# Optimization experiments

Hardware: AMD Instinct MI355X
Metric: run time of the kernel (lower is better)

The kernel has to match this reference:

```python
import jax, jax.numpy as jnp
from jax import lax
import numpy as np

# dims (match init_kwargs config)
B, L, D = 32, 512, 32          # batch, seq_len, input_dim
H = 256                         # hidden_dim
E = 8                           # num_experts
PLEN, O = 96, 32                # pred_len, output_dim
LAT = 256                       # flow latent_dim
PD, NPROT = 64, 16              # prototype_dim, num_prototypes


def setup_inputs() -> dict:
    key = jax.random.key(0)
    ks = iter(jax.random.split(key, 40))
    def n(shape, scale=0.02):
        return (jax.random.normal(next(ks), shape, jnp.float32) * scale)
    inp = {
        'x': jax.random.normal(next(ks), (B, L, D), jnp.float32),
        # prototypes + projector (metric gating / diversity)
        'prototypes': n((NPROT, PD), 0.5),
        'Wp': n((PD, PD)), 'bp': jnp.zeros((PD,), jnp.float32),
        # expert_feature_extractor: Linear(7D->H), ReLU, Linear(H->PD), LayerNorm(PD)
        'Wf1': n((7 * D, H)), 'bf1': jnp.zeros((H,), jnp.float32),
        'Wf2': n((H, PD)), 'bf2': jnp.zeros((PD,), jnp.float32),
        'ln_g': jnp.ones((PD,), jnp.float32), 'ln_b': jnp.zeros((PD,), jnp.float32),
        # flow encoder (latent mapping of flattened window) + gating head
        'W1': n((L * D, H)), 'b1': jnp.zeros((H,), jnp.float32),
        'W2': n((H, LAT)), 'b2': jnp.zeros((LAT,), jnp.float32),
        'Wg': n((LAT, E)), 'bg': jnp.zeros((E,), jnp.float32),
        'log_temp': jnp.zeros((), jnp.float32),
        # stacked FFT+Mamba expert params (leading axis = expert)
        'Win': n((E, D, H)), 'b_in': jnp.zeros((E, H), jnp.float32),
        'Wfft': n((E, H, H)), 'b_fft': jnp.zeros((E, H), jnp.float32),
        'a_logit': n((E, H), 1.0),
        'Whead': n((E, H, PLEN * O)), 'b_head': jnp.zeros((E, PLEN * O), jnp.float32),
    }
    return inp


def _expert_features(x, Wf1, bf1, Wf2, bf2, ln_g, ln_b):
    # faithful to compute_expert_features: 7 per-channel stats -> MLP -> LayerNorm
    Lf = jnp.float32(x.shape[1])
    x_mean = x.mean(axis=1)
    x_std = x.std(axis=1, ddof=1)             # torch unbiased std
    x_min = x.min(axis=1)
    x_max = x.max(axis=1)
    x_diff_mean = jnp.diff(x, axis=1).mean(axis=1)
    x_trend = (x[:, -1, :] - x[:, 0, :]) / Lf
    x_fft_mag = jnp.abs(jnp.fft.fft(x, axis=1)).mean(axis=1)
    cf = jnp.concatenate([x_mean, x_std, x_min, x_max, x_diff_mean, x_trend, x_fft_mag], axis=1)
    h = jax.nn.relu(cf @ Wf1 + bf1)
    ef = h @ Wf2 + bf2
    mu = ef.mean(axis=-1, keepdims=True)
    var = ef.var(axis=-1, keepdims=True)
    return (ef - mu) / jnp.sqrt(var + 1e-5) * ln_g + ln_b


def reference(x, prototypes, Wp, bp, Wf1, bf1, Wf2, bf2, ln_g, ln_b,
              W1, b1, W2, b2, Wg, bg, log_temp,
              Win, b_in, Wfft, b_fft, a_logit, Whead, b_head):
    b, l, d = x.shape
    # --- metric-based gating ---
    ef = _expert_features(x, Wf1, bf1, Wf2, bf2, ln_g, ln_b)           # [B,PD]
    latent = jax.nn.relu(x.reshape(b, -1) @ W1 + b1) @ W2 + b2          # flow latent [B,LAT]
    lg = latent @ Wg + bg                                               # [B,E]
    proj = ef @ Wp + bp                                                 # prototype_projector
    d2 = ((proj[:, None, :] - prototypes[None, :, :]) ** 2).sum(-1)     # [B,NPROT]
    d2_per_expert = d2.reshape(b, E, NPROT // E).min(axis=-1)           # min dist to each expert's prototypes
    temp = jnp.clip(jnp.exp(log_temp), 0.1, 10.0)
    w = jax.nn.softmax((lg - d2_per_expert) / temp, axis=-1)            # [B,E]

    # --- FFT + Mamba-style experts (vmapped over stacked expert params) ---
    def expert(Win_e, b_in_e, Wfft_e, b_fft_e, a_logit_e, Whead_e, b_head_e):
        h = jnp.einsum('bld,dh->blh', x, Win_e) + b_in_e                # [B,L,H]
        f = jnp.einsum('blh,hk->blk', jnp.abs(jnp.fft.fft(h, axis=1)), Wfft_e) + b_fft_e
        u = jax.nn.relu(h + f)
        a = jax.nn.sigmoid(a_logit_e)                                   # per-channel decay
        def step(s, ut):
            s = a * s + (1.0 - a) * ut
            return s, None
        s_last, _ = lax.scan(step, jnp.zeros((b, H), x.dtype), jnp.swapaxes(u, 0, 1))
        return (s_last @ Whead_e + b_head_e).reshape(b, PLEN, O)

    outs = jax.vmap(expert)(Win, b_in, Wfft, b_fft, a_logit, Whead, b_head)  # [E,B,PLEN,O]
    y = jnp.einsum('be,ebpo->bpo', w, outs)
    return y
```

## Files before the change

### kernel.cpp

```cpp
#include <hip/hip_runtime.h>
#include <hip/hip_bf16.h>


typedef __hip_bfloat16 bf16;
typedef unsigned short u16;
typedef __attribute__((ext_vector_type(8))) short s8v;
typedef __attribute__((ext_vector_type(4))) float f4v;

#define MFMA_BF16(a,b,c) __builtin_amdgcn_mfma_f32_16x16x32_bf16(a,b,c,0,0,0)

#if __has_builtin(__builtin_amdgcn_sqrtf)
#define FSQRT(x) __builtin_amdgcn_sqrtf(x)
#else
#define FSQRT(x) sqrtf(x)
#endif
#if __has_builtin(__builtin_amdgcn_exp2f)
#define FEXP2(x) __builtin_amdgcn_exp2f(x)
#else
#define FEXP2(x) exp2f(x)
#endif
#if __has_builtin(__builtin_amdgcn_logf)
#define FLOG2(x) __builtin_amdgcn_logf(x)
#else
#define FLOG2(x) log2f(x)
#endif

#define GWF1 0
#define GW2  57344
#define GWF2 122880
#define GWP  139264
#define GPROT 143360
#define GWG  144384

__device__ __forceinline__ float bf2f(u16 u){
  union{ unsigned u32; float f; } w; w.u32 = ((unsigned)u) << 16; return w.f;
}
__device__ __forceinline__ u16 f2bf(float f){
  bf16 h = __float2bfloat16(f);
  union{ bf16 b; u16 u; } w; w.b = h; return w.u;
}
__device__ __forceinline__ u16 f2bf_fast(float f){
  union{ float f; unsigned u; } v; v.f = f;
  unsigned r = v.u + 0x7FFFu + ((v.u >> 16) & 1u);
  return (u16)(r >> 16);
}
__device__ __forceinline__ float ldg_(const void* p, long long i, bool bf){
  float r;
  if(bf) r = bf2f(((const u16*)p)[i]);
  else   r = ((const float*)p)[i];
  return r;
}
__device__ __forceinline__ bool bfflag(const void* ln_g){
  return ((const u16*)ln_g)[0] == 0x3F80;
}

__global__ __launch_bounds__(256) void ks1(const void* __restrict__ ln_g,
    const void* __restrict__ x,
    const void* __restrict__ Win, const void* __restrict__ Wfft,
    const void* __restrict__ W1, const void* __restrict__ Whead,
    const void* __restrict__ Wf1, const void* __restrict__ W2,
    const void* __restrict__ Wf2, const void* __restrict__ Wp,
    const void* __restrict__ prot, const void* __restrict__ Wg,
    u16* __restrict__ xbf,
    u16* __restrict__ WinTg, u16* __restrict__ WfftTg,
    u16* __restrict__ W1Tg, u16* __restrict__ WheadTg,
    u16* __restrict__ gw,
    u16* __restrict__ Xr, u16* __restrict__ Xi, float* __restrict__ cf){
  const bool bf = bfflag(ln_g);
  __shared__ float xs[512], re[512], im[512];
  __shared__ float twr[256], twi[256];
  __shared__ float r0s[4], r1s[4], r2s[4], r3s[4];
  __shared__ u16 tile[64][72];
  int BX = blockIdx.x, t = threadIdx.x;

  if(BX < 1024){
    int b = BX >> 5, d = BX & 31;
    {
      float rev = -(float)t * (1.f/512.f);
#if __has_builtin(__builtin_amdgcn_cosf) && __has_builtin(__builtin_amdgcn_sinf)
      twr[t] = __builtin_amdgcn_cosf(rev);
      twi[t] = __builtin_amdgcn_sinf(rev);
#else
      float ang = rev * 6.283185307179586f;
      twr[t] = cosf(ang); twi[t] = sinf(ang);
#endif
    }
    for(int i=t;i<512;i+=256){
      float v = ldg_(x, (long long)(b*512+i)*32 + d, bf);
      xs[i] = v;
      re[__brev((unsigned)i) >> 23] = v;
      im[i] = 0.f;
    }
    __syncthreads();
    float s=0.f, s2=0.f, mn=3.0e38f, mx=-3.0e38f;
    for(int i=t;i<512;i+=256){ float v=xs[i]; s+=v; s2+=v*v; mn=fminf(mn,v); mx=fmaxf(mx,v); }
    #pragma unroll
    for(int o=32;o>0;o>>=1){
      s  += __shfl_down(s,o);  s2 += __shfl_down(s2,o);
      mn = fminf(mn,__shfl_down(mn,o)); mx = fmaxf(mx,__shfl_down(mx,o));
    }
    int wv = t>>6, ln = t&63;
    if(ln==0){ r0s[wv]=s; r1s[wv]=s2; r2s[wv]=mn; r3s[wv]=mx; }
    __syncthreads();
    if(t==0){
      float S =r0s[0]+r0s[1]+r0s[2]+r0s[3];
      float S2=r1s[0]+r1s[1]+r1s[2]+r1s[3];
      float MN=fminf(fminf(r2s[0],r2s[1]),fminf(r2s[2],r2s[3]));
      float MX=fmaxf(fmaxf(r3s[0],r3s[1]),fmaxf(r3s[2],r3s[3]));
      float mean = S*(1.f/512.f);
      float var  = (S2 - S*S*(1.f/512.f))*(1.f/511.f);
      float* c = cf + b*224;
      c[d]      = mean;
      c[32+d]   = sqrtf(fmaxf(var,0.f));
      c[64+d]   = MN;
      c[96+d]   = MX;
      float dv = xs[511]-xs[0];
      c[128+d]  = dv*(1.f/511.f);
      c[160+d]  = dv*(1.f/512.f);
    }
    for(int st=1; st<=9; ++st){
      __syncthreads();
      int m = 1<<st, half = m>>1;
      int grp = t >> (st-1);
      int k   = t & (half-1);
      int i1 = grp*m + k, i2 = i1 + half;
      int ti_ = k << (9-st);
      float cs = twr[ti_], sn = twi[ti_];
      float ar=re[i1], ai=im[i1], br=re[i2], bi=im[i2];
      float tr = cs*br - sn*bi;
      float ti = cs*bi + sn*br;
      re[i1]=ar+tr; im[i1]=ai+ti;
      re[i2]=ar-tr; im[i2]=ai-ti;
    }
    __syncthreads();
    float ms=0.f;
    for(int i=t;i<512;i+=256){
      float rr=re[i], ii=im[i];
      if(i <= 256){
        long long o = (long long)(b*512+i)*32 + d;
        Xr[o]=f2bf(rr); Xi[o]=f2bf(ii);
      }
      ms += FSQRT(rr*rr+ii*ii);
    }
    #pragma unroll
    for(int o=32;o>0;o>>=1) ms += __shfl_down(ms,o);
    if(ln==0) r0s[wv]=ms;
    __syncthreads();
    if(t==0) cf[b*224 + 192 + d] = (r0s[0]+r0s[1]+r0s[2]+r0s[3])*(1.f/512.f);
    return;
  }
  if(BX < 4111){
    int bx = BX - 1024;
    if(bx < 256){
      int i = bx*256 + t;
      int e = i >> 13, r = i & 8191;
      int c = r >> 5, d = r & 31;
      WinTg[i] = f2bf(ldg_(Win, (long long)e*8192 + d*256 + c, bf));
      return;
    }
    if(bx < 384){
      int idx = bx - 256;
      int e = idx >> 4, tl = idx & 15, kb = tl >> 2, cb = tl & 3;
      if(bf){
        for(int q=0;q<16;q++){
          int G = q*256 + t; int ki = G >> 6, ci = G & 63;
          tile[ci][ki] = ((const u16*)Wfft)[(long long)e*65536 + (long long)(kb*64+ki)*256 + cb*64+ci];
        }
      } else {
        for(int q=0;q<16;q++){
          int G = q*256 + t; int ki = G >> 6, ci = G & 63;
          tile[ci][ki] = f2bf(((const float*)Wfft)[(long long)e*65536 + (long long)(kb*64+ki)*256 + cb*64+ci]);
        }
      }
      __syncthreads();
      for(int q=0;q<16;q++){
        int G = q*256 + t; int ci = G >> 6, ki = G & 63;
        WfftTg[(long long)e*65536 + (long long)(cb*64+ci)*256 + kb*64+ki] = tile[ci][ki];
      }
      return;
    }
    if(bx < 1408){
      int idx = bx - 384;
      int kb = idx & 255, nb = idx >> 8;
      if(bf){
        for(int q=0;q<16;q++){
          int G = q*256 + t; int ki = G >> 6, ni = G & 63;
          tile[ni][ki] = ((const u16*)W1)[(long long)(kb*64+ki)*256 + nb*64+ni];
        }
      } else {
        for(int q=0;q<16;q++){
          int G = q*256 + t; int ki = G >> 6, ni = G & 63;
          tile[ni][ki] = f2bf(((const float*)W1)[(long long)(kb*64+ki)*256 + nb*64+ni]);
        }
      }
      __syncthreads();
      for(int q=0;q<16;q++){
        int G = q*256 + t; int ni = G >> 6, ki = G & 63;
        W1Tg[(long long)(nb*64+ni)*16384 + kb*64+ki] = tile[ni][ki];
      }
      return;
    }
    if(bx < 2944){
      int idx = bx - 1408;
      int e = idx / 192, rem = idx % 192;
      int kb = rem / 48, nb = rem % 48;
      if(bf){
        for(int q=0;q<16;q++){
          int G = q*256 + t; int ki = G >> 6, ni = G & 63;
          tile[ni][ki] = ((const u16*)Whead)[(long long)e*786432 + (long long)(kb*64+ki)*3072 + nb*64+ni];
        }
      } else {
        for(int q=0;q<16;q++){
          int G = q*256 + t; int ki = G >> 6, ni = G & 63;
          tile[ni][ki] = f2bf(((const float*)Whead)[(long long)e*786432 + (long long)(kb*64+ki)*3072 + nb*64+ni]);
        }
      }
      __syncthreads();
      for(int q=0;q<16;q++){
        int G = q*256 + t; int ni = G >> 6, ki = G & 63;
        WheadTg[(long long)e*786432 + (long long)(nb*64+ni)*256 + kb*64+ki] = tile[ni][ki];
      }
      return;
    }
    {
      int c = bx - 2944;
      const void* src; int dstbase, blkoff;
      if(c < 56)      { src=Wf1;  dstbase=GWF1;  blkoff=c; }
      else if(c <120) { src=W2;   dstbase=GW2;   blkoff=c-56; }
      else if(c <136) { src=Wf2;  dstbase=GWF2;  blkoff=c-120; }
      else if(c <140) { src=Wp;   dstbase=GWP;   blkoff=c-136; }
      else if(c <141) { src=prot; dstbase=GPROT; blkoff=0; }
      else            { src=Wg;   dstbase=GWG;   blkoff=c-141; }
      int i = blkoff*1024 + t*4;
      if(bf){
        ushort4 v = *(const ushort4*)((const u16*)src + i);
        *(ushort4*)(gw + dstbase + i) = v;
      } else {
        float4 f = *(const float4*)((const float*)src + i);
        ushort4 v; v.x=f2bf(f.x); v.y=f2bf(f.y); v.z=f2bf(f.z); v.w=f2bf(f.w);
        *(ushort4*)(gw + dstbase + i) = v;
      }
    }
    return;
  }
  {
    int i = ((BX-4111)*256 + t)*4;
    if(bf){
      ushort4 v = *(const ushort4*)((const u16*)x + i);
      *(ushort4*)(xbf+i) = v;
    } else {
      float4 f = *(const float4*)((const float*)x + i);
      ushort4 v; v.x=f2bf(f.x); v.y=f2bf(f.y); v.z=f2bf(f.z); v.w=f2bf(f.w);
      *(ushort4*)(xbf+i) = v;
    }
  }
}

__global__ __launch_bounds__(256) void ks2(const void* __restrict__ ln_g,
    const u16* __restrict__ xbf, const u16* __restrict__ Xr, const u16* __restrict__ Xi,
    const u16* __restrict__ WinTg, const u16* __restrict__ W1Tg,
    const u16* __restrict__ gw, const float* __restrict__ cf,
    const void* __restrict__ bf1, const void* __restrict__ b_in,
    const void* __restrict__ b_fft, const void* __restrict__ a_logit,
    const void* __restrict__ Win, const void* __restrict__ Wfft,
    float* __restrict__ psum, u16* __restrict__ hmagG,
    float* __restrict__ h1f, float* __restrict__ contrib){
  const bool bf = bfflag(ln_g);
  int BX = blockIdx.x, t = threadIdx.x;
  int w = t >> 6, lane = t & 63, quad = lane >> 4, l15 = lane & 15;
  const f4v zf = (f4v){0.f,0.f,0.f,0.f};
  __shared__ float binS[256];
  __shared__ float cfs[224];
  __shared__ float hm[256];
  __shared__ float xr6[32], xi6[32], x6[32];

  if(BX < 64){
    int kb = BX;
    f4v acc[2][4];
    #pragma unroll
    for(int mt=0;mt<2;mt++)
      #pragma unroll
      for(int nt=0;nt<4;nt++) acc[mt][nt] = zf;
    #pragma unroll
    for(int ks=0;ks<8;ks++){
      long long k = kb*256 + ks*32 + quad*8;
      s8v aF[2], bF[4];
      #pragma unroll
      for(int mt=0;mt<2;mt++)
        aF[mt] = *(const s8v*)(xbf + (long long)(mt*16 + l15)*16384 + k);
      #pragma unroll
      for(int nt=0;nt<4;nt++)
        bF[nt] = *(const s8v*)(W1Tg + (long long)(w*64 + nt*16 + l15)*16384 + k);
      #pragma unroll
      for(int mt=0;mt<2;mt++)
        #pragma unroll
        for(int nt=0;nt<4;nt++)
          acc[mt][nt] = MFMA_BF16(aF[mt], bF[nt], acc[mt][nt]);
    }
    float* po = psum + (long long)kb*8192;
    #pragma unroll
    for(int mt=0;mt<2;mt++)
      #pragma unroll
      for(int nt=0;nt<4;nt++)
        #pragma unroll
        for(int r=0;r<4;r++)
          po[(mt*16 + quad*4 + r)*256 + w*64 + nt*16 + l15] = acc[mt][nt][r];
    return;
  }
  if(BX < 1088){
    int bx = BX - 64;
    int e = bx >> 7, inner = bx & 127;
    int b = inner >> 2, half = (inner >> 1) & 1, kh = inner & 1;
    int row0 = b*512 + half*128;
    binS[t] = ldg_(b_in, e*256+t, bf);
    s8v xrF[2], xiF[2];
    #pragma unroll
    for(int nt=0;nt<2;nt++){
      long long row = row0 + w*32 + nt*16 + l15;
      xrF[nt] = *(const s8v*)(Xr + row*32 + quad*8);
      xiF[nt] = *(const s8v*)(Xi + row*32 + quad*8);
    }
    __syncthreads();
    u16* Ho = hmagG + (long long)((e<<6)|(b<<1)|half)*32768;
    #pragma unroll
    for(int kcl=0;kcl<2;kcl++){
      int k0 = (kh*2+kcl)*64;
      #pragma unroll
      for(int ct=0;ct<4;ct++){
        s8v wfr = *(const s8v*)(WinTg + ((long long)e*256 + k0 + ct*16 + l15)*32 + quad*8);
        #pragma unroll
        for(int nt=0;nt<2;nt++){
          f4v hr = MFMA_BF16(wfr, xrF[nt], zf);
          f4v hi = MFMA_BF16(wfr, xiF[nt], zf);
          int rowg = row0 + w*32 + nt*16 + l15;
          bool bin0 = ((rowg & 511) == 0);
          ushort4 pk;
          int cb4 = k0 + ct*16 + quad*4;
          float h0 = hr[0] + (bin0 ? 512.f*binS[cb4+0] : 0.f);
          float h1 = hr[1] + (bin0 ? 512.f*binS[cb4+1] : 0.f);
          float h2 = hr[2] + (bin0 ? 512.f*binS[cb4+2] : 0.f);
          float h3 = hr[3] + (bin0 ? 512.f*binS[cb4+3] : 0.f);
          pk.x = f2bf_fast(FSQRT(h0*h0 + hi[0]*hi[0]));
          pk.y = f2bf_fast(FSQRT(h1*h1 + hi[1]*hi[1]));
          pk.z = f2bf_fast(FSQRT(h2*h2 + hi[2]*hi[2]));
          pk.w = f2bf_fast(FSQRT(h3*h3 + hi[3]*hi[3]));
          *(ushort4*)&Ho[(w*32 + nt*16 + l15)*256 + cb4] = pk;
        }
      }
    }
    return;
  }
  if(BX < 1120){
    int b = BX - 1088;
    if(t < 224) cfs[t] = cf[(long long)b*224 + t];
    __syncthreads();
    float a1 = ldg_(bf1, t, bf);
    const u16* Wp_ = gw + GWF1 + t;
    #pragma unroll 16
    for(int k=0;k<224;k++) a1 += cfs[k]*bf2f(Wp_[k*256]);
    h1f[b*256+t] = fmaxf(a1, 0.f);
    return;
  }
  {
    int bx = BX - 1120;
    int e = bx >> 5, b = bx & 31, j = t;
    if(j < 32){
      long long o = ((long long)(b*512 + 256))*32 + j;
      xr6[j] = bf2f(Xr[o]);
      xi6[j] = bf2f(Xi[o]);
      x6[j]  = bf2f(xbf[o]);
    }
    __syncthreads();
    float sr=0.f, si=0.f, hx=0.f;
    if(bf){
      const u16* Wn = (const u16*)Win + (long long)e*8192 + j;
      #pragma unroll 8
      for(int d=0; d<32; d++){
        float wv = bf2f(Wn[d*256]);
        sr += xr6[d]*wv; si += xi6[d]*wv; hx += x6[d]*wv;
      }
    } else {
      const float* Wn = (const float*)Win + (long long)e*8192 + j;
      #pragma unroll 8
      for(int d=0; d<32; d++){
        float wv = Wn[d*256];
        sr += xr6[d]*wv; si += xi6[d]*wv; hx += x6[d]*wv;
      }
    }
    hm[j] = FSQRT(sr*sr + si*si);
    __syncthreads();
    float f = 0.f;
    if(bf){
      const u16* Wf = (const u16*)Wfft + (long long)e*65536 + j;
      #pragma unroll 8
      for(int k=0;k<256;k++) f += hm[k]*bf2f(Wf[(long long)k*256]);
    } else {
      const float* Wf = (const float*)Wfft + (long long)e*65536 + j;
      #pragma unroll 8
      for(int k=0;k<256;k++) f += hm[k]*Wf[(long long)k*256];
    }
    float a = 1.f/(1.f+__expf(-ldg_(a_logit, e*256+j, bf)));
    a = fminf(fmaxf(a, 1e-12f), 0.99999988f);
    float l2a = FLOG2(a);
    float u = fmaxf(hx + f + ldg_(b_in,e*256+j,bf) + ldg_(b_fft,e*256+j,bf), 0.f);
    contrib[(e*32+b)*256 + j] = u * FEXP2(l2a * 255.f);
  }
}

__global__ __launch_bounds__(256) void ks3(const void* __restrict__ ln_g,
    const float* __restrict__ psum, const float* __restrict__ h1f,
    const u16* __restrict__ gw,
    const void* __restrict__ b1, const void* __restrict__ bf2,
    const void* __restrict__ ln_b, const void* __restrict__ bp,
    const void* __restrict__ b2, const void* __restrict__ bg,
    const void* __restrict__ log_temp,
    const u16* __restrict__ xbf, const u16* __restrict__ hmagG,
    const u16* __restrict__ WinTg, const u16* __restrict__ WfftTg,
    const void* __restrict__ b_in, const void* __restrict__ b_fft,
    const void* __restrict__ a_logit,
    float* __restrict__ wgt, float* __restrict__ sp){
  const bool bf = bfflag(ln_g);
  int BX = blockIdx.x, t = threadIdx.x;
  __shared__ __align__(16) u16 BsT[128][72];
  __shared__ float biasS[128], l2aS[128], aS[128];
  __shared__ float hsL[256], h1L[256], latL[256], efL[64], prL[64];
  __shared__ float red[4][64];
  __shared__ float d2part[16][16], d2s[16], lgpart[32][8];

  if(BX < 32){
    int b = BX;
    {
      float s0=0.f, s1=0.f, s2=0.f, s3=0.f;
      #pragma unroll
      for(int kb=0;kb<64;kb+=4){
        s0 += psum[(long long)(kb+0)*8192 + b*256 + t];
        s1 += psum[(long long)(kb+1)*8192 + b*256 + t];
        s2 += psum[(long long)(kb+2)*8192 + b*256 + t];
        s3 += psum[(long long)(kb+3)*8192 + b*256 + t];
      }
      hsL[t] = fmaxf((s0+s1)+(s2+s3) + ldg_(b1,t,bf), 0.f);
    }
    h1L[t] = h1f[b*256+t];
    __syncthreads();
    {
      float a = ldg_(b2, t, bf);
      const u16* W2p = gw + GW2 + t;
      #pragma unroll 16
      for(int k=0;k<256;k++) a += hsL[k]*bf2f(W2p[k*256]);
      latL[t] = a;
    }
    {
      int p = t>>6, j = t&63;
      float acc = 0.f;
      const u16* Wf2p = gw + GWF2 + p*64*64 + j;
      #pragma unroll 16
      for(int i=0;i<64;i++) acc += h1L[p*64+i]*bf2f(Wf2p[i*64]);
      red[p][j] = acc;
    }
    __syncthreads();
    if(t < 64){
      float a2 = red[0][t]+red[1][t]+red[2][t]+red[3][t] + ldg_(bf2,t,bf);
      float sm=a2, sq=a2*a2;
      #pragma unroll
      for(int o=32;o>0;o>>=1){ sm += __shfl_xor(sm,o); sq += __shfl_xor(sq,o); }
      float mu  = sm*(1.f/64.f);
      float var = sq*(1.f/64.f) - mu*mu;
      efL[t] = (a2-mu)*rsqrtf(fmaxf(var,0.f)+1e-5f)*ldg_(ln_g,t,bf) + ldg_(ln_b,t,bf);
      float p_acc = ldg_(bp, t, bf);
      const u16* Wpp = gw + GWP + t;
      #pragma unroll 16
      for(int k=0;k<64;k++) p_acc += efL[k]*bf2f(Wpp[k*64]);
      prL[t] = p_acc;
    }
    {
      int part = t>>3, e = t&7;
      float gp = 0.f;
      const u16* Wgp = gw + GWG + e;
      #pragma unroll
      for(int i=0;i<8;i++){
        int k = part*8 + i;
        gp += latL[k]*bf2f(Wgp[k*8]);
      }
      lgpart[part][e] = gp;
    }
    __syncthreads();
    {
      int p = t>>4, q4 = t&15;
      float dd = 0.f;
      #pragma unroll
      for(int i=0;i<4;i++){
        int d = q4*4 + i;
        float df = prL[d] - bf2f(gw[GPROT + p*64 + d]);
        dd += df*df;
      }
      d2part[p][q4] = dd;
    }
    __syncthreads();
    if(t < 16){
      float s = 0.f;
      #pragma unroll
      for(int i=0;i<16;i++) s += d2part[t][i];
      d2s[t] = s;
    }
    __syncthreads();
    if(t < 8){
      float g = ldg_(bg, t, bf);
      #pragma unroll
      for(int p=0;p<32;p++) g += lgpart[p][t];
      float d2pe = fminf(d2s[2*t], d2s[2*t+1]);
      float temp = fminf(fmaxf(__expf(ldg_(log_temp,0,bf)), 0.1f), 10.f);
      float v = (g - d2pe) / temp;
      float m = v;
      m = fmaxf(m, __shfl_xor(m,1));
      m = fmaxf(m, __shfl_xor(m,2));
      m = fmaxf(m, __shfl_xor(m,4));
      float ex = __expf(v-m);
      float sum = ex;
      sum += __shfl_xor(sum,1);
      sum += __shfl_xor(sum,2);
      sum += __shfl_xor(sum,4);
      wgt[b*8+t] = ex/sum;
    }
    return;
  }
  {
    int bx = BX - 32;
    int e = bx >> 7, inner = bx & 127;
    int b = inner >> 2, half = (inner >> 1) & 1, cb = inner & 1;
    int row0 = b*512 + half*128;
    int col0 = cb*128;
    int w = t >> 6, lane = t & 63, quad = lane >> 4, l15 = lane & 15;

    if(t < 128){
      int c = col0 + t;
      biasS[t] = ldg_(b_in, e*256+c, bf) + ldg_(b_fft, e*256+c, bf);
      float a = 1.f/(1.f+__expf(-ldg_(a_logit, e*256+c, bf)));
      a = fminf(fmaxf(a, 1e-12f), 0.99999988f);
      aS[t] = a;
      l2aS[t] = FLOG2(a);
    }
    const u16* Ab = hmagG + (long long)((e<<6)|(b<<1)|half)*32768;
    const f4v zf = (f4v){0.f,0.f,0.f,0.f};
    f4v acc[2][8];
    #pragma unroll
    for(int mt=0;mt<2;mt++)
      #pragma unroll
      for(int nt=0;nt<8;nt++) acc[mt][nt] = zf;

    for(int kc=0;kc<4;kc++){
      int k0 = kc*64;
      __syncthreads();
      #pragma unroll
      for(int q=0;q<4;q++){
        int G = q*256 + t;
        int c = G >> 3, k8 = (G & 7)*8;
        *(s8v*)&BsT[c][k8] = *(const s8v*)(WfftTg + ((long long)e*256 + col0 + c)*256 + k0 + k8);
      }
      __syncthreads();
      #pragma unroll
      for(int ks=0;ks<2;ks++){
        int kb = ks*32 + quad*8;
        s8v aF0 = *(const s8v*)(Ab + (w*32 + l15)*256 + k0 + kb);
        s8v aF1 = *(const s8v*)(Ab + (w*32 + 16 + l15)*256 + k0 + kb);
        #pragma unroll
        for(int nt=0;nt<8;nt++){
          s8v bF = *(const s8v*)&BsT[nt*16 + l15][kb];
          acc[0][nt] = MFMA_BF16(aF0, bF, acc[0][nt]);
          acc[1][nt] = MFMA_BF16(aF1, bF, acc[1][nt]);
        }
      }
    }
    s8v xF[2], xFm[2];
    #pragma unroll
    for(int mt=0;mt<2;mt++){
      long long rowO = (long long)row0 + w*32 + mt*16 + l15;
      xF[mt] = *(const s8v*)(xbf + rowO*32 + quad*8);
      int lin = half*128 + w*32 + mt*16 + l15;
      int lm  = (512 - lin) & 511;
      xFm[mt] = *(const s8v*)(xbf + ((long long)b*512 + lm)*32 + quad*8);
    }
    int l0base = half*128 + w*32 + quad*4;
    float mz = (l0base == 0) ? 0.f : 1.f;
    const f4v zf2 = (f4v){0.f,0.f,0.f,0.f};
    float part[8];
    #pragma unroll
    for(int nt=0;nt<8;nt++){
      s8v wfh = *(const s8v*)(WinTg + ((long long)e*256 + col0 + nt*16 + l15)*32 + quad*8);
      f4v hv0 = MFMA_BF16(xF[0],  wfh, zf2);
      f4v hv1 = MFMA_BF16(xF[1],  wfh, zf2);
      f4v hm0 = MFMA_BF16(xFm[0], wfh, zf2);
      f4v hm1 = MFMA_BF16(xFm[1], wfh, zf2);
      int cl = nt*16 + l15;
      float l2a = l2aS[cl], bias = biasS[cl], av = aS[cl];
      float inv_a = FEXP2(-l2a);
      float cO0 = FEXP2(l2a * (float)(511 - l0base));
      float cO1 = FEXP2(l2a * (float)(495 - l0base));
      float cM0 = FEXP2(l2a * (float)(l0base - 1));
      float cM1 = FEXP2(l2a * (float)(l0base + 15));
      float sum = 0.f;
      #pragma unroll
      for(int r=0;r<4;r++){
        float u0 = fmaxf(acc[0][nt][r] + hv0[r] + bias, 0.f);
        sum += u0 * cO0;
        float u1 = fmaxf(acc[1][nt][r] + hv1[r] + bias, 0.f);
        sum += u1 * cO1;
        float m0 = fmaxf(acc[0][nt][r] + hm0[r] + bias, 0.f);
        float w0 = m0 * cM0;
        if(r == 0) w0 *= mz;
        sum += w0;
        float m1 = fmaxf(acc[1][nt][r] + hm1[r] + bias, 0.f);
        sum += m1 * cM1;
        cO0 *= inv_a; cO1 *= inv_a; cM0 *= av; cM1 *= av;
      }
      part[nt] = sum;
    }
    __syncthreads();
    float (*redS)[132] = (float(*)[132])BsT;
    #pragma unroll
    for(int nt=0;nt<8;nt++)
      redS[w*4 + quad][nt*16 + l15] = part[nt];
    __syncthreads();
    if(t < 128){
      float tot = 0.f;
      #pragma unroll
      for(int i=0;i<16;i++) tot += redS[i][t];
      sp[e*16384 + (b*2 + half)*256 + col0 + t] = tot;
    }
  }
}

__global__ __launch_bounds__(256) void k6_mfma(const void* __restrict__ ln_g,
    const float* __restrict__ sp, const float* __restrict__ contrib,
    const void* __restrict__ a_logit,
    const u16* __restrict__ WheadTg, float* __restrict__ yaccE){
  const bool bf = bfflag(ln_g);
  int nb = blockIdx.x, e = blockIdx.y;
  int t = threadIdx.x;
  int w = t >> 6, lane = t & 63, quad = lane >> 4, l15 = lane & 15;
  __shared__ __align__(16) u16 ssS[32][264];
  {
    float a = 1.f/(1.f+__expf(-ldg_(a_logit, e*256+t, bf)));
    a = fminf(fmaxf(a, 1e-12f), 0.99999988f);
    float oma = 1.f - a;
    const float* sp0 = sp + e*16384 + t;
    const float* cb  = contrib + e*8192 + t;
    #pragma unroll
    for(int q=0;q<32;q++){
      float v = oma*(sp0[q*512] + sp0[q*512+256] + cb[q*256]);
      ssS[q][t] = f2bf(v);
    }
  }
  __syncthreads();
  const f4v zf = (f4v){0.f,0.f,0.f,0.f};
  f4v acc[2][2];
  #pragma unroll
  for(int mt=0;mt<2;mt++)
    #pragma unroll
    for(int nt=0;nt<2;nt++) acc[mt][nt] = zf;
  #pragma unroll
  for(int ks=0;ks<8;ks++){
    int k = ks*32 + quad*8;
    s8v aF0 = *(const s8v*)&ssS[l15][k];
    s8v aF1 = *(const s8v*)&ssS[16 + l15][k];
    s8v bF[2];
    #pragma unroll
    for(int nt=0;nt<2;nt++)
      bF[nt] = *(const s8v*)(WheadTg + ((long long)e*3072 + nb*128 + w*32 + nt*16 + l15)*256 + k);
    acc[0][0] = MFMA_BF16(aF0, bF[0], acc[0][0]);
    acc[0][1] = MFMA_BF16(aF0, bF[1], acc[0][1]);
    acc[1][0] = MFMA_BF16(aF1, bF[0], acc[1][0]);
    acc[1][1] = MFMA_BF16(aF1, bF[1], acc[1][1]);
  }
  float* yo = yaccE + (long long)e*98304;
  #pragma unroll
  for(int mt=0;mt<2;mt++)
    #pragma unroll
    for(int nt=0;nt<2;nt++){
      int col = nb*128 + w*32 + nt*16 + l15;
      #pragma unroll
      for(int r=0;r<4;r++){
        int b = mt*16 + quad*4 + r;
        yo[b*3072 + col] = acc[mt][nt][r];
      }
    }
}

__global__ void k7_out(const void* __restrict__ ln_g,
                       const float* __restrict__ yaccE,
                       const float* __restrict__ wgt,
                       const void* __restrict__ b_head,
                       void* __restrict__ out){
  const bool bf = bfflag(ln_g);
  int i = blockIdx.x*256 + threadIdx.x;
  int b = i / 3072, col = i - b*3072;
  float v = 0.f;
  #pragma unroll
  for(int e=0;e<8;e++)
    v += wgt[b*8+e]*(yaccE[(long long)e*98304 + i] + ldg_(b_head, (long long)e*3072+col, bf));
  if(bf) ((u16*)out)[i] = f2bf(v);
  else   ((float*)out)[i] = v;
}

extern "C" void kernel_launch(void* const* d_in, const int* in_sizes, int n_in,
                              void* d_out, int out_size, void* d_ws, size_t ws_size,
                              hipStream_t stream){
  const void* x       = d_in[0];
  const void* prot    = d_in[1];
  const void* Wp      = d_in[2];
  const void* bp      = d_in[3];
  const void* Wf1     = d_in[4];
  const void* bf1     = d_in[5];
  const void* Wf2     = d_in[6];
  const void* bf2     = d_in[7];
  const void* ln_g    = d_in[8];
  const void* ln_b    = d_in[9];
  const void* W1      = d_in[10];
  const void* b1      = d_in[11];
  const void* W2      = d_in[12];
  const void* b2      = d_in[13];
  const void* Wg      = d_in[14];
  const void* bg      = d_in[15];
  const void* log_temp= d_in[16];
  const void* Win     = d_in[17];
  const void* b_in    = d_in[18];
  const void* Wfft    = d_in[19];
  const void* b_fft   = d_in[20];
  const void* a_logit = d_in[21];
  const void* Whead   = d_in[22];
  const void* b_head  = d_in[23];

  float* ws      = (float*)d_ws;
  float* cf      = ws;
  float* wgt     = cf + 7168;
  float* sp      = wgt + 256;
  float* h1f     = sp + 131072;
  float* contrib = h1f + 8192;
  float* psum    = contrib + 65536;
  float* yaccE   = psum + 524288;
  u16*   Xr      = (u16*)(yaccE + 786432);
  u16*   Xi      = Xr + 524288;
  u16*   xbf     = Xi + 524288;
  u16*   WinTg   = xbf + 524288;
  u16*   WfftTg  = WinTg + 65536;
  u16*   W1Tg    = WfftTg + 524288;
  u16*   WheadTg = W1Tg + 4194304;
  u16*   gw      = WheadTg + 6291456;
  u16*   hmagG   = gw + 146432;

  ks1 <<<dim3(4623), dim3(256), 0, stream>>>(ln_g, x, Win, Wfft, W1, Whead,
                                             Wf1, W2, Wf2, Wp, prot, Wg,
                                             xbf, WinTg, WfftTg, W1Tg, WheadTg, gw,
                                             Xr, Xi, cf);
  ks2 <<<dim3(1376), dim3(256), 0, stream>>>(ln_g, xbf, Xr, Xi, WinTg, W1Tg,
                                             gw, cf, bf1, b_in, b_fft, a_logit,
                                             Win, Wfft,
                                             psum, hmagG, h1f, contrib);
  ks3 <<<dim3(1056), dim3(256), 0, stream>>>(ln_g, psum, h1f, gw,
                                             b1, bf2, ln_b, bp, b2, bg, log_temp,
                                             xbf, hmagG, WinTg, WfftTg,
                                             b_in, b_fft, a_logit,
                                             wgt, sp);
  k6_mfma <<<dim3(24,8), dim3(256), 0, stream>>>(ln_g, sp, contrib, a_logit,
                                                 WheadTg, yaccE);
  k7_out  <<<dim3(384),  dim3(256), 0, stream>>>(ln_g, yaccE, wgt, b_head, d_out);
}
```

Baseline: 196.1 us.

## Fuse expert-weighted output reduction into head GEMM via atomics and last-block finalize

Removes the separate k7_out kernel by having each k6 block atomically accumulate gate-weighted head outputs (plus bias) into a single yacc buffer. A per-column-block counter lets the last of the 8 expert blocks write the final output. Zeroing of yacc and the counters is folded into extra blocks of ks3. This saves one launch and the per-expert intermediate buffer, at the cost of float atomics, which make the summation order nondeterministic.

Result: slower. 205.6 us (+4.9%).

```diff
diff --git a/kernel.cpp b/kernel.cpp
--- a/kernel.cpp
+++ b/kernel.cpp
@@ -418,7 +418,8 @@
     const u16* __restrict__ WinTg, const u16* __restrict__ WfftTg,
     const void* __restrict__ b_in, const void* __restrict__ b_fft,
     const void* __restrict__ a_logit,
-    float* __restrict__ wgt, float* __restrict__ sp){
+    float* __restrict__ wgt, float* __restrict__ sp,
+    float* __restrict__ yacc, int* __restrict__ done){
   const bool bf = bfflag(ln_g);
   int BX = blockIdx.x, t = threadIdx.x;
   __shared__ __align__(16) u16 BsT[128][72];
@@ -427,6 +428,12 @@
   __shared__ float red[4][64];
   __shared__ float d2part[16][16], d2s[16], lgpart[32][8];
 
+  if(BX >= 1056){
+    int idx = (BX-1056)*256 + t;
+    if(idx < 24576) *(float4*)(yacc + idx*4) = (float4){0.f,0.f,0.f,0.f};
+    if(BX == 1056 && t < 32) done[t] = 0;
+    return;
+  }
   if(BX < 32){
     int b = BX;
     {
@@ -631,13 +638,18 @@
 
 __global__ __launch_bounds__(256) void k6_mfma(const void* __restrict__ ln_g,
     const float* __restrict__ sp, const float* __restrict__ contrib,
-    const void* __restrict__ a_logit,
-    const u16* __restrict__ WheadTg, float* __restrict__ yaccE){
+    const float* __restrict__ wgt, const void* __restrict__ a_logit,
+    const u16* __restrict__ WheadTg, const void* __restrict__ b_head,
+    float* __restrict__ yacc, int* __restrict__ done,
+    void* __restrict__ out){
   const bool bf = bfflag(ln_g);
   int nb = blockIdx.x, e = blockIdx.y;
   int t = threadIdx.x;
   int w = t >> 6, lane = t & 63, quad = lane >> 4, l15 = lane & 15;
   __shared__ __align__(16) u16 ssS[32][264];
+  __shared__ float wgtS[256];
+  __shared__ int sdone;
+  wgtS[t] = wgt[t];
   {
     float a = 1.f/(1.f+__expf(-ldg_(a_logit, e*256+t, bf)));
     a = fminf(fmaxf(a, 1e-12f), 0.99999988f);
@@ -671,34 +683,35 @@
     acc[1][0] = MFMA_BF16(aF1, bF[0], acc[1][0]);
     acc[1][1] = MFMA_BF16(aF1, bF[1], acc[1][1]);
   }
-  float* yo = yaccE + (long long)e*98304;
   #pragma unroll
-  for(int mt=0;mt<2;mt++)
-    #pragma unroll
-    for(int nt=0;nt<2;nt++){
-      int col = nb*128 + w*32 + nt*16 + l15;
+  for(int nt=0;nt<2;nt++){
+    int col = nb*128 + w*32 + nt*16 + l15;
+    float bh = ldg_(b_head, (long long)e*3072 + col, bf);
+    #pragma unroll
+    for(int mt=0;mt<2;mt++)
       #pragma unroll
       for(int r=0;r<4;r++){
         int b = mt*16 + quad*4 + r;
-        yo[b*3072 + col] = acc[mt][nt][r];
-      }
-    }
-}
-
-__global__ void k7_out(const void* __restrict__ ln_g,
-                       const float* __restrict__ yaccE,
-                       const float* __restrict__ wgt,
-                       const void* __restrict__ b_head,
-                       void* __restrict__ out){
-  const bool bf = bfflag(ln_g);
-  int i = blockIdx.x*256 + threadIdx.x;
-  int b = i / 3072, col = i - b*3072;
-  float v = 0.f;
-  #pragma unroll
-  for(int e=0;e<8;e++)
-    v += wgt[b*8+e]*(yaccE[(long long)e*98304 + i] + ldg_(b_head, (long long)e*3072+col, bf));
-  if(bf) ((u16*)out)[i] = f2bf(v);
-  else   ((float*)out)[i] = v;
+        atomicAdd(&yacc[b*3072 + col], wgtS[b*8+e]*(acc[mt][nt][r] + bh));
+      }
+  }
+  __syncthreads();
+  if(t == 0){
+    __threadfence();
+    sdone = (atomicAdd(&done[nb], 1) == 7);
+  }
+  __syncthreads();
+  if(sdone){
+    #pragma unroll
+    for(int q=0;q<16;q++){
+      int idx = q*256 + t;
+      int b = idx >> 7, c = idx & 127;
+      long long o = (long long)b*3072 + nb*128 + c;
+      float v = atomicAdd(&yacc[o], 0.f);
+      if(bf) ((u16*)out)[o] = f2bf(v);
+      else   ((float*)out)[o] = v;
+    }
+  }
 }
 
 extern "C" void kernel_launch(void* const* d_in, const int* in_sizes, int n_in,
@@ -736,8 +749,9 @@
   float* h1f     = sp + 131072;
   float* contrib = h1f + 8192;
   float* psum    = contrib + 65536;
-  float* yaccE   = psum + 524288;
-  u16*   Xr      = (u16*)(yaccE + 786432);
+  float* yacc    = psum + 524288;
+  int*   done    = (int*)(yacc + 98304);
+  u16*   Xr      = (u16*)(done + 32);
   u16*   Xi      = Xr + 524288;
   u16*   xbf     = Xi + 524288;
   u16*   WinTg   = xbf + 524288;
@@ -755,12 +769,11 @@
                                              gw, cf, bf1, b_in, b_fft, a_logit,
                                              Win, Wfft,
                                              psum, hmagG, h1f, contrib);
-  ks3 <<<dim3(1056), dim3(256), 0, stream>>>(ln_g, psum, h1f, gw,
+  ks3 <<<dim3(1153), dim3(256), 0, stream>>>(ln_g, psum, h1f, gw,
                                              b1, bf2, ln_b, bp, b2, bg, log_temp,
                                              xbf, hmagG, WinTg, WfftTg,
                                              b_in, b_fft, a_logit,
-                                             wgt, sp);
-  k6_mfma <<<dim3(24,8), dim3(256), 0, stream>>>(ln_g, sp, contrib, a_logit,
-                                                 WheadTg, yaccE);
-  k7_out  <<<dim3(384),  dim3(256), 0, stream>>>(ln_g, yaccE, wgt, b_head, d_out);
-}
+                                             wgt, sp, yacc, done);
+  k6_mfma <<<dim3(24,8), dim3(256), 0, stream>>>(ln_g, sp, contrib, wgt, a_logit,
+                                                 WheadTg, b_head, yacc, done, d_out);
+}
```
